# Kernel tuning notes

Hardware: AMD Instinct MI355X
Metric: run time of the kernel (lower is better)

The kernel has to match this reference:

```python
import jax, jax.numpy as jnp
import numpy as np

B, NQ, NM, NHR, D, H, FF = 16, 100, 5440, 4096, 256, 8, 2048

def _ln(x, w, b):
    m = x.mean(-1, keepdims=True)
    v = ((x - m) ** 2).mean(-1, keepdims=True)
    return (x - m) * jax.lax.rsqrt(v + 1e-5) * w + b

def setup_inputs():
    key = jax.random.key(0)
    ks = iter(jax.random.split(key, 32))
    def rn(shape, s=1.0):
        return jax.random.normal(next(ks), shape, jnp.float32) * s
    return {
        'tgt': rn((B, NQ, D)),
        'memory': rn((B, NM, D)),
        'memory_hr': rn((B, NHR, D)),
        'prior_attn_bias': rn((B, NQ, NM)),
        'query_pos': rn((B, NQ, D)),
        'ln_cross_w': jnp.ones((D,)), 'ln_cross_b': jnp.zeros((D,)),
        'q_w': rn((D, D), 0.02), 'q_b': jnp.zeros((D,)),
        'k_w': rn((D, D), 0.02), 'k_b': jnp.zeros((D,)),
        'v_w': rn((D, D), 0.02), 'v_b': jnp.zeros((D,)),
        'out_w': rn((D, D), 0.02), 'out_b': jnp.zeros((D,)),
        'ln_self_w': jnp.ones((D,)), 'ln_self_b': jnp.zeros((D,)),
        'sa_in_w': rn((3 * D, D), 0.02), 'sa_in_b': jnp.zeros((3 * D,)),
        'sa_out_w': rn((D, D), 0.02), 'sa_out_b': jnp.zeros((D,)),
        'ln_ffn_w': jnp.ones((D,)), 'ln_ffn_b': jnp.zeros((D,)),
        'lin1_w': rn((FF, D), 0.02), 'lin1_b': jnp.zeros((FF,)),
        'lin2_w': rn((D, FF), 0.02), 'lin2_b': jnp.zeros((D,)),
        'me_w': rn((D, D), 0.02), 'me_b': jnp.zeros((D,)),
    }

def reference(tgt, memory, memory_hr, prior_attn_bias, query_pos,
              ln_cross_w, ln_cross_b, q_w, q_b, k_w, k_b, v_w, v_b,
              out_w, out_b, ln_self_w, ln_self_b, sa_in_w, sa_in_b,
              sa_out_w, sa_out_b, ln_ffn_w, ln_ffn_b, lin1_w, lin1_b,
              lin2_w, lin2_b, me_w, me_b):
    b, nq, d = tgt.shape
    nm = memory.shape[1]
    h = H
    dh = d // h
    scale = dh ** -0.5
    # ---- cross-attention with additive prior bias (eval mode: dropout = id) ----
    x = _ln(tgt, ln_cross_w, ln_cross_b)
    q = ((x + query_pos) @ q_w.T + q_b).reshape(b, nq, h, dh)
    k = (memory @ k_w.T + k_b).reshape(b, nm, h, dh)
    v = (memory @ v_w.T + v_b).reshape(b, nm, h, dh)
    attn = jnp.einsum('bqhd,bmhd->bhqm', q, k) * scale + prior_attn_bias[:, None]  # [b,h,nq,nm]
    a = jax.nn.softmax(attn, axis=-1)
    o = jnp.einsum('bhqm,bmhd->bqhd', a, v).reshape(b, nq, d)
    tgt = tgt + (o @ out_w.T + out_b)
    # ---- self-attention (torch nn.MultiheadAttention, batch_first, eval) ----
    z = _ln(tgt, ln_self_w, ln_self_b)
    zq = z + query_pos
    qs = (zq @ sa_in_w[:d].T + sa_in_b[:d]).reshape(b, nq, h, dh)
    ks = (zq @ sa_in_w[d:2 * d].T + sa_in_b[d:2 * d]).reshape(b, nq, h, dh)
    vs = (z @ sa_in_w[2 * d:].T + sa_in_b[2 * d:]).reshape(b, nq, h, dh)
    sattn = jax.nn.softmax(jnp.einsum('bqhd,bmhd->bhqm', qs, ks) * scale, axis=-1)
    so = jnp.einsum('bhqm,bmhd->bqhd', sattn, vs).reshape(b, nq, d)
    tgt = tgt + (so @ sa_out_w.T + sa_out_b)
    # ---- FFN ----
    y = _ln(tgt, ln_ffn_w, ln_ffn_b)
    y = jax.nn.gelu(y @ lin1_w.T + lin1_b, approximate=False) @ lin2_w.T + lin2_b
    tgt = tgt + y
    # ---- mask branch ----
    mask_logits = jnp.einsum('bqd,bmd->bqm', tgt @ me_w.T + me_b, memory_hr)
    return (tgt, mask_logits)
```

## Files before the change

### kernel.cpp

```cpp
#include <hip/hip_runtime.h>

typedef unsigned short u16;
typedef unsigned int u32;
typedef __bf16 bf16x8 __attribute__((ext_vector_type(8)));
typedef float f32x4 __attribute__((ext_vector_type(4)));

__device__ __forceinline__ u16 f2b(float f) {
  u32 u = __float_as_uint(f);
  u32 r = (u + 0x7fffu + ((u >> 16) & 1u)) >> 16;
  return (u16)r;
}
__device__ __forceinline__ float b2f(u16 h) {
  return __uint_as_float(((u32)h) << 16);
}
__device__ __forceinline__ bf16x8 zero8() {
  union { uint4 u; bf16x8 v; } z; z.u = make_uint4(0u, 0u, 0u, 0u); return z.v;
}
__device__ __forceinline__ u32 cvtpk(float lo, float hi) {
  u32 r;
  asm("v_cvt_pk_bf16_f32 %0, %1, %2" : "=v"(r) : "v"(lo), "v"(hi));
  return r;
}

struct Seg { const float* in; u16* out; int n4; };
struct PrepArgs {
  Seg seg[7];
  const float *k_w, *v_w, *k_b, *v_b, *pbias;
  u16 *Wf, *biasT;
  float *kvB;
};

__global__ __launch_bounds__(256)
void prep_kernel(PrepArgs a)
{
  __shared__ float S[100][69];
  const int bx = blockIdx.x, tid = threadIdx.x;
  if (bx < 1472) {
    int bxr = bx;
#pragma unroll
    for (int k = 0; k < 7; ++k) {
      const int nb = a.seg[k].n4 >> 8;
      if (bxr < nb) {
        const int i = bxr * 256 + tid;
        const float4 f = *(const float4*)(a.seg[k].in + (size_t)i * 4);
        uint2 pk; pk.x = cvtpk(f.x, f.y); pk.y = cvtpk(f.z, f.w);
        *(uint2*)(a.seg[k].out + (size_t)i * 4) = pk;
        return;
      }
      bxr -= nb;
    }
    return;
  } else if (bx < 1536) {
    const int i = bx - 1472, gI = i >> 3, ks = i & 7;
    const int nt = tid >> 6, lane = tid & 63, lr = lane & 15, g = lane >> 4;
    const float* src = (gI < 4 ? a.k_w + (size_t)(gI * 64 + nt * 16 + lr) * 256
                               : a.v_w + (size_t)((gI - 4) * 64 + nt * 16 + lr) * 256)
                       + ks * 32 + g * 8;
    const float4 f0 = *(const float4*)src;
    const float4 f1 = *(const float4*)(src + 4);
    uint4 pk;
    pk.x = cvtpk(f0.x, f0.y); pk.y = cvtpk(f0.z, f0.w);
    pk.z = cvtpk(f1.x, f1.y); pk.w = cvtpk(f1.z, f1.w);
    *(uint4*)(a.Wf + (size_t)((gI * 8 + ks) * 4 + nt) * 512 + lane * 8) = pk;
  } else if (bx < 1538) {
    const int i = (bx - 1536) * 256 + tid;
    a.kvB[i] = (i < 256) ? a.k_b[i] : a.v_b[i - 256];
  } else {
    const int bt = bx - 1538;
    const int b = bt / 85, m0 = (bt - b * 85) * 64;
    for (int idx = tid; idx < 1600; idx += 256) {
      const int q = idx >> 4, seg = idx & 15;
      const float4 v = *(const float4*)(a.pbias + (size_t)(b * 100 + q) * 5440 + m0 + seg * 4);
      S[q][seg * 4 + 0] = v.x; S[q][seg * 4 + 1] = v.y;
      S[q][seg * 4 + 2] = v.z; S[q][seg * 4 + 3] = v.w;
    }
    __syncthreads();
    for (int idx = tid; idx < 1792; idx += 256) {
      const int m = idx / 28, qg = (idx % 28) * 4;
      u16 h[4];
#pragma unroll
      for (int r = 0; r < 4; ++r) {
        const int q = qg + r;
        h[r] = (q < 100) ? f2b(S[q][m]) : (u16)0;
      }
      uint2 pk;
      pk.x = (u32)h[0] | ((u32)h[1] << 16);
      pk.y = (u32)h[2] | ((u32)h[3] << 16);
      *(uint2*)(a.biasT + ((size_t)(b * 5440 + m0 + m)) * 112 + qg) = pk;
    }
  }
}

template<int ROWS>
__device__ __forceinline__ void ln_stage(const float* __restrict__ x, int row0,
    const float* __restrict__ w, const float* __restrict__ b,
    const float* __restrict__ pos, u16* As)
{
  const int tid = threadIdx.x, lane = tid & 63, wid = tid >> 6;
  const float4 wv = *(const float4*)(w + lane * 4);
  const float4 bv = *(const float4*)(b + lane * 4);
#pragma unroll
  for (int rr = 0; rr < ROWS / 4; ++rr) {
    const int rl = wid * (ROWS / 4) + rr;
    const size_t o = (size_t)(row0 + rl) * 256 + lane * 4;
    const float4 v = *(const float4*)(x + o);
    float s = v.x + v.y + v.z + v.w;
#pragma unroll
    for (int m = 1; m < 64; m <<= 1) s += __shfl_xor(s, m);
    const float mean = s * (1.f / 256.f);
    const float d0 = v.x - mean, d1 = v.y - mean, d2 = v.z - mean, d3 = v.w - mean;
    float ss = d0 * d0 + d1 * d1 + d2 * d2 + d3 * d3;
#pragma unroll
    for (int m = 1; m < 64; m <<= 1) ss += __shfl_xor(ss, m);
    const float rs = rsqrtf(ss * (1.f / 256.f) + 1e-5f);
    float y0 = d0 * rs * wv.x + bv.x;
    float y1 = d1 * rs * wv.y + bv.y;
    float y2 = d2 * rs * wv.z + bv.z;
    float y3 = d3 * rs * wv.w + bv.w;
    if (pos) {
      const float4 pv = *(const float4*)(pos + o);
      y0 += pv.x; y1 += pv.y; y2 += pv.z; y3 += pv.w;
    }
    uint2 pk; pk.x = cvtpk(y0, y1); pk.y = cvtpk(y2, y3);
    const int byte = (rl * 512 + lane * 8) ^ ((rl & 7) << 4);
    *(uint2*)((char*)As + byte) = pk;
  }
}

__device__ __forceinline__ void gemm16x128(const u16* As, const u16* __restrict__ W,
                                           u16 (*Ws)[40], f32x4 acc[2])
{
  const int tid = threadIdx.x, lane = tid & 63, wid = tid >> 6;
  const int g = lane >> 4, lr = lane & 15;
  for (int k0 = 0; k0 < 256; k0 += 32) {
    for (int cid = tid; cid < 512; cid += 256) {
      const int r = cid >> 2, cg = (cid & 3) * 8;
      *(uint4*)&Ws[r][cg] = *(const uint4*)(W + (size_t)r * 256 + k0 + cg);
    }
    __syncthreads();
    const int abyte = (lr * 512 + k0 * 2 + g * 16) ^ ((lr & 7) << 4);
    const bf16x8 af = *(const bf16x8*)((const char*)As + abyte);
#pragma unroll
    for (int nt = 0; nt < 2; ++nt) {
      const bf16x8 bfr = *(const bf16x8*)&Ws[wid * 32 + nt * 16 + lr][g * 8];
      acc[nt] = __builtin_amdgcn_mfma_f32_16x16x32_bf16(af, bfr, acc[nt], 0, 0, 0);
    }
    __syncthreads();
  }
}

__global__ __launch_bounds__(256)
void qproj_kernel(const float* __restrict__ x, const float* __restrict__ lnw,
                  const float* __restrict__ lnb, const float* __restrict__ pos,
                  const u16* __restrict__ W, const float* __restrict__ bias,
                  u16* __restrict__ out, float scale)
{
  __shared__ u16 As[16 * 256];
  __shared__ u16 Ws[128][40];
  const int tid = threadIdx.x, lane = tid & 63, wid = tid >> 6;
  const int g = lane >> 4, lr = lane & 15;
  const int row0 = blockIdx.x * 16, n0 = blockIdx.y * 128;
  ln_stage<16>(x, row0, lnw, lnb, pos, As);
  f32x4 acc[2] = {};
  gemm16x128(As, W + (size_t)n0 * 256, Ws, acc);
#pragma unroll
  for (int nt = 0; nt < 2; ++nt) {
    const int col = n0 + wid * 32 + nt * 16 + lr;
    const float bv = bias[col];
#pragma unroll
    for (int r = 0; r < 4; ++r) {
      const int row = row0 + g * 4 + r;
      out[(size_t)row * 256 + col] = f2b((acc[nt][r] + bv) * scale);
    }
  }
}

__global__ __launch_bounds__(256)
void sain_kernel(const float* __restrict__ x, const float* __restrict__ lnw,
                 const float* __restrict__ lnb, const float* __restrict__ pos,
                 const u16* __restrict__ W, const float* __restrict__ bias,
                 float* __restrict__ qkb, float* __restrict__ vsb)
{
  __shared__ u16 As[16 * 256];
  __shared__ u16 Ws[128][40];
  const int tid = threadIdx.x, lane = tid & 63, wid = tid >> 6;
  const int g = lane >> 4, lr = lane & 15;
  const int row0 = blockIdx.x * 16, y = blockIdx.y;
  ln_stage<16>(x, row0, lnw, lnb, (y < 4) ? pos : nullptr, As);
  f32x4 acc[2] = {};
  gemm16x128(As, W + (size_t)y * 128 * 256, Ws, acc);
#pragma unroll
  for (int nt = 0; nt < 2; ++nt) {
    const int cl = wid * 32 + nt * 16 + lr;
    const float bv = bias[y * 128 + cl];
#pragma unroll
    for (int r = 0; r < 4; ++r) {
      const int row = row0 + g * 4 + r;
      const float v = acc[nt][r] + bv;
      if (y < 4) qkb[(size_t)row * 512 + y * 128 + cl] = v;
      else       vsb[(size_t)row * 256 + (y - 4) * 128 + cl] = v;
    }
  }
}

__global__ __launch_bounds__(256)
void ffn1_kernel(const float* __restrict__ x, const float* __restrict__ lnw,
                 const float* __restrict__ lnb, const u16* __restrict__ W,
                 const float* __restrict__ bias, u16* __restrict__ out)
{
  __shared__ u16 As[64 * 256];
  __shared__ u16 Ws[256][40];
  const int tid = threadIdx.x, lane = tid & 63, wid = tid >> 6;
  const int g = lane >> 4, lr = lane & 15;
  const int row0 = blockIdx.x * 64, n0 = blockIdx.y * 256;
  ln_stage<64>(x, row0, lnw, lnb, nullptr, As);
  f32x4 acc[16] = {};
  for (int k0 = 0; k0 < 256; k0 += 32) {
    for (int cid = tid; cid < 1024; cid += 256) {
      const int r = cid >> 2, cg = (cid & 3) * 8;
      *(uint4*)&Ws[r][cg] = *(const uint4*)(W + (size_t)(n0 + r) * 256 + k0 + cg);
    }
    __syncthreads();
    const int arow = wid * 16 + lr;
    const int abyte = (arow * 512 + k0 * 2 + g * 16) ^ ((arow & 7) << 4);
    const bf16x8 af = *(const bf16x8*)((const char*)As + abyte);
#pragma unroll
    for (int nt = 0; nt < 16; ++nt) {
      const bf16x8 bfr = *(const bf16x8*)&Ws[nt * 16 + lr][g * 8];
      acc[nt] = __builtin_amdgcn_mfma_f32_16x16x32_bf16(af, bfr, acc[nt], 0, 0, 0);
    }
    __syncthreads();
  }
#pragma unroll
  for (int nt = 0; nt < 16; ++nt) {
    const int col = n0 + nt * 16 + lr;
    const float bv = bias[col];
#pragma unroll
    for (int r = 0; r < 4; ++r) {
      const int row = row0 + wid * 16 + g * 4 + r;
      float v = acc[nt][r] + bv;
      v = 0.5f * v * (1.f + erff(v * 0.70710678118654752f));
      out[(size_t)row * 2048 + col] = f2b(v);
    }
  }
}

template<int BM, int BN, int WM, int WN, int GELU_, int RES_, int OF32, int OBF>
__global__ __launch_bounds__(256)
void gemm_kernel(const u16* __restrict__ Ap, const u16* __restrict__ W,
                 const float* __restrict__ bias, const float* __restrict__ res,
                 float* __restrict__ Cf, u16* __restrict__ Cb,
                 int M, int N, int K, float scale)
{
  constexpr int WROWS = BM / WM;
  constexpr int WCOLS = BN / WN;
  constexpr int MT = WROWS / 16;
  constexpr int NT = WCOLS / 16;
  static_assert(WM * WN == 4, "4 waves");
  __shared__ u16 As[BM][40];
  __shared__ u16 Ws[BN][40];
  const int tid = threadIdx.x, lane = tid & 63, wid = tid >> 6;
  const int g = lane >> 4, lr = lane & 15;
  const int m0 = blockIdx.x * BM, n0 = blockIdx.y * BN;
  const int wm = wid / WN, wn = wid % WN;
  f32x4 acc[MT][NT] = {};
  for (int k0 = 0; k0 < K; k0 += 32) {
    for (int cid = tid; cid < BM * 4; cid += 256) {
      int r = cid >> 2, cg = (cid & 3) * 8;
      *(uint4*)&As[r][cg] = *(const uint4*)(Ap + (size_t)(m0 + r) * K + k0 + cg);
    }
    for (int cid = tid; cid < BN * 4; cid += 256) {
      int r = cid >> 2, cg = (cid & 3) * 8;
      *(uint4*)&Ws[r][cg] = *(const uint4*)(W + (size_t)(n0 + r) * K + k0 + cg);
    }
    __syncthreads();
    bf16x8 af[MT], bfr[NT];
#pragma unroll
    for (int mt = 0; mt < MT; ++mt) af[mt] = *(const bf16x8*)&As[wm * WROWS + mt * 16 + lr][g * 8];
#pragma unroll
    for (int nt = 0; nt < NT; ++nt) bfr[nt] = *(const bf16x8*)&Ws[wn * WCOLS + nt * 16 + lr][g * 8];
#pragma unroll
    for (int mt = 0; mt < MT; ++mt)
#pragma unroll
      for (int nt = 0; nt < NT; ++nt)
        acc[mt][nt] = __builtin_amdgcn_mfma_f32_16x16x32_bf16(af[mt], bfr[nt], acc[mt][nt], 0, 0, 0);
    __syncthreads();
  }
#pragma unroll
  for (int mt = 0; mt < MT; ++mt)
#pragma unroll
    for (int nt = 0; nt < NT; ++nt) {
      const int col = n0 + wn * WCOLS + nt * 16 + lr;
      const float bv = bias[col];
#pragma unroll
      for (int r = 0; r < 4; ++r) {
        const int row = m0 + wm * WROWS + mt * 16 + g * 4 + r;
        float v = (acc[mt][nt][r] + bv) * scale;
        if constexpr (GELU_) v = 0.5f * v * (1.f + erff(v * 0.70710678118654752f));
        if constexpr (RES_) v += res[(size_t)row * N + col];
        if constexpr (OF32) Cf[(size_t)row * N + col] = v;
        if constexpr (OBF) Cb[(size_t)row * N + col] = f2b(v);
      }
    }
}

__global__ __launch_bounds__(512, 4)
void kv_gemm_kernel(const float* __restrict__ A, const u16* __restrict__ Wf,
                    const float* __restrict__ biasKV,
                    u16* __restrict__ Kb, u16* __restrict__ Vt)
{
  __shared__ u16 As[64 * 256];
  const int tid = threadIdx.x, lane = tid & 63, wid = tid >> 6;
  const int g = lane >> 4, lr = lane & 15;
  const int bidx = blockIdx.x / 85, t = blockIdx.x - bidx * 85;
  const int row0 = blockIdx.x * 64;

  for (int ch = tid; ch < 2048; ch += 512) {
    const int r = ch >> 5, c8 = (ch & 31) * 8;
    const float* ap = A + (size_t)(row0 + r) * 256 + c8;
    const float4 f0 = *(const float4*)ap;
    const float4 f1 = *(const float4*)(ap + 4);
    uint4 pk;
    pk.x = cvtpk(f0.x, f0.y);
    pk.y = cvtpk(f0.z, f0.w);
    pk.z = cvtpk(f1.x, f1.y);
    pk.w = cvtpk(f1.z, f1.w);
    const int byte = r * 512 + c8 * 2;
    *(uint4*)((char*)As + (byte ^ ((r & 7) << 4))) = pk;
  }
  __syncthreads();

  const u16* wbase = Wf + (size_t)wid * 8 * 4 * 512 + lane * 8;
  f32x4 acc[4][4] = {};
#pragma unroll 2
  for (int ks = 0; ks < 8; ++ks) {
    bf16x8 bfv[4], af[4];
#pragma unroll
    for (int nt = 0; nt < 4; ++nt)
      bfv[nt] = *(const bf16x8*)(wbase + (ks * 4 + nt) * 512);
#pragma unroll
    for (int mt = 0; mt < 4; ++mt) {
      const int r = mt * 16 + lr;
      const int byte = r * 512 + ks * 64 + g * 16;
      af[mt] = *(const bf16x8*)((const char*)As + (byte ^ ((r & 7) << 4)));
    }
#pragma unroll
    for (int mt = 0; mt < 4; ++mt)
#pragma unroll
      for (int nt = 0; nt < 4; ++nt)
        acc[mt][nt] = __builtin_amdgcn_mfma_f32_16x16x32_bf16(af[mt], bfv[nt], acc[mt][nt], 0, 0, 0);
  }
  __syncthreads();

  const int isV = wid >> 2;
  if (isV) {
#pragma unroll
    for (int nt = 0; nt < 4; ++nt) {
      const int col = (wid - 4) * 64 + nt * 16 + lr;
      const float bv = biasKV[256 + col];
#pragma unroll
      for (int mt = 0; mt < 4; ++mt)
#pragma unroll
        for (int r = 0; r < 4; ++r) {
          const int slot = (mt >> 1) * 32 + 8 * g + 2 * r + (mt & 1);
          const int byte = (col * 128 + slot * 2) ^ ((col & 7) << 4);
          *(u16*)((char*)As + byte) = f2b(acc[mt][nt][r] + bv);
        }
    }
  }
  __syncthreads();
  {
    const size_t vbase = (size_t)bidx * 256 * 5440 + (size_t)t * 64;
#pragma unroll
    for (int p = 0; p < 4; ++p) {
      const int idx = p * 512 + tid;
      const int col = idx >> 3, chunk = idx & 7;
      const int lbyte = col * 128 + ((chunk * 16) ^ ((col & 7) << 4));
      const uint4 v = *(const uint4*)((const char*)As + lbyte);
      *(uint4*)(Vt + vbase + (size_t)col * 5440 + chunk * 8) = v;
    }
  }
  __syncthreads();
  if (!isV) {
#pragma unroll
    for (int nt = 0; nt < 4; ++nt) {
      const int col = wid * 64 + nt * 16 + lr;
      const float bv = biasKV[col];
#pragma unroll
      for (int mt = 0; mt < 4; ++mt)
#pragma unroll
        for (int r = 0; r < 4; ++r) {
          const int row = mt * 16 + g * 4 + r;
          const int byte = (row * 512 + col * 2) ^ ((row & 7) << 4);
          *(u16*)((char*)As + byte) = f2b(acc[mt][nt][r] + bv);
        }
    }
  }
  __syncthreads();
#pragma unroll
  for (int p = 0; p < 4; ++p) {
    const int idx = p * 512 + tid;
    const int row = idx >> 5, c16 = idx & 31;
    const int lbyte = row * 512 + ((c16 * 16) ^ ((row & 7) << 4));
    const uint4 v = *(const uint4*)((const char*)As + lbyte);
    *(uint4*)(Kb + (size_t)(row0 + row) * 256 + c16 * 8) = v;
  }
}

__global__ __launch_bounds__(256, 3)
void cross_attn_kernel(const u16* __restrict__ Q, const u16* __restrict__ Kb,
                       const u16* __restrict__ Vt, const u16* __restrict__ biasT,
                       float* __restrict__ Opart, float* __restrict__ ML)
{
  __shared__ u32 P32[4][112][20];
  const int tid = threadIdx.x, lane = tid & 63, wid = tid >> 6;
  const int g = lane >> 4, lr = lane & 15;
  const int b = blockIdx.y, c = blockIdx.x;
  const int head = blockIdx.z * 4 + wid;
  const int m_base = c * 320;
  const f32x4 zf = {0.f, 0.f, 0.f, 0.f};

  bf16x8 qf[7];
#pragma unroll
  for (int mt = 0; mt < 7; ++mt) {
    int qr = mt * 16 + lr;
    qf[mt] = (qr < 100) ? *(const bf16x8*)&Q[(size_t)(b * 100 + qr) * 256 + head * 32 + g * 8]
                        : zero8();
  }
  float Mst[7];
  f32x4 Lp[7];
  f32x4 Oa[7][2];
#pragma unroll
  for (int mt = 0; mt < 7; ++mt) { Mst[mt] = -1e30f; Lp[mt] = zf; Oa[mt][0] = zf; Oa[mt][1] = zf; }

  for (int s = 0; s < 10; ++s) {
    const int m0 = m_base + s * 32;
    const bf16x8 kf0 = *(const bf16x8*)&Kb[(size_t)(b * 5440 + m0 + lr) * 256 + head * 32 + g * 8];
    const bf16x8 kf1 = *(const bf16x8*)&Kb[(size_t)(b * 5440 + m0 + 16 + lr) * 256 + head * 32 + g * 8];
    const size_t vrow = ((size_t)(b * 8 + head) * 32 + lr) * 5440 + m0 + g * 8;
    const bf16x8 vf0 = *(const bf16x8*)&Vt[vrow];
    const bf16x8 vf1 = *(const bf16x8*)&Vt[vrow + 16 * 5440];
    const u16* bb = biasT + ((size_t)(b * 5440 + m0 + lr)) * 112 + g * 4;
#pragma unroll
    for (int mt = 0; mt < 7; ++mt) {
      f32x4 s0 = __builtin_amdgcn_mfma_f32_16x16x32_bf16(qf[mt], kf0, zf, 0, 0, 0);
      f32x4 s1 = __builtin_amdgcn_mfma_f32_16x16x32_bf16(qf[mt], kf1, zf, 0, 0, 0);
      const uint2 b0 = *(const uint2*)(bb + mt * 16);
      const uint2 b1 = *(const uint2*)(bb + 16 * 112 + mt * 16);
      s0[0] += b2f((u16)b0.x);      s0[1] += b2f((u16)(b0.x >> 16));
      s0[2] += b2f((u16)b0.y);      s0[3] += b2f((u16)(b0.y >> 16));
      s1[0] += b2f((u16)b1.x);      s1[1] += b2f((u16)(b1.x >> 16));
      s1[2] += b2f((u16)b1.y);      s1[3] += b2f((u16)(b1.y >> 16));
      float mx = fmaxf(fmaxf(fmaxf(s0[0], s0[1]), fmaxf(s0[2], s0[3])),
                       fmaxf(fmaxf(s1[0], s1[1]), fmaxf(s1[2], s1[3])));
#pragma unroll
      for (int d = 1; d < 16; d <<= 1) mx = fmaxf(mx, __shfl_xor(mx, d, 16));
      const float newM = fmaxf(Mst[mt], mx);
      const float al = __expf(Mst[mt] - newM);
      Mst[mt] = newM;
      f32x4 p0, p1;
#pragma unroll
      for (int r = 0; r < 4; ++r) {
        p0[r] = __expf(s0[r] - newM);
        p1[r] = __expf(s1[r] - newM);
      }
      Lp[mt] = Lp[mt] * al + (p0 + p1);
      Oa[mt][0] *= al;
      Oa[mt][1] *= al;
#pragma unroll
      for (int r = 0; r < 4; ++r)
        P32[wid][mt * 16 + g * 4 + r][lr] = (u32)f2b(p0[r]) | ((u32)f2b(p1[r]) << 16);
    }
#pragma unroll
    for (int mt = 0; mt < 7; ++mt) {
      const bf16x8 pa = *(const bf16x8*)&P32[wid][mt * 16 + lr][g * 4];
      Oa[mt][0] = __builtin_amdgcn_mfma_f32_16x16x32_bf16(pa, vf0, Oa[mt][0], 0, 0, 0);
      Oa[mt][1] = __builtin_amdgcn_mfma_f32_16x16x32_bf16(pa, vf1, Oa[mt][1], 0, 0, 0);
    }
  }
  const int bh = b * 8 + head;
#pragma unroll
  for (int mt = 0; mt < 7; ++mt)
#pragma unroll
    for (int r = 0; r < 4; ++r) {
      const int qr = mt * 16 + g * 4 + r;
      if (qr < 100) {
        float L = Lp[mt][r];
#pragma unroll
        for (int d = 1; d < 16; d <<= 1) L += __shfl_xor(L, d, 16);
        const size_t rb = (size_t)(bh * 17 + c) * 100 + qr;
        Opart[rb * 32 + lr] = Oa[mt][0][r];
        Opart[rb * 32 + 16 + lr] = Oa[mt][1][r];
        if (lr == 0) { ML[rb * 2] = Mst[mt]; ML[rb * 2 + 1] = L; }
      }
    }
}

__global__ __launch_bounds__(256)
void reduce_attn_kernel(const float* __restrict__ Opart, const float* __restrict__ ML,
                        u16* __restrict__ outb)
{
  const int row = blockIdx.x;
  const int b = row / 100, q = row % 100;
  const int h = threadIdx.x >> 5, d = threadIdx.x & 31;
  const int bh = b * 8 + h;
  float gm = -1e30f;
  for (int c = 0; c < 17; ++c) gm = fmaxf(gm, ML[((size_t)(bh * 17 + c) * 100 + q) * 2]);
  float l = 0.f, o = 0.f;
  for (int c = 0; c < 17; ++c) {
    const size_t rb = (size_t)(bh * 17 + c) * 100 + q;
    const float w = __expf(ML[rb * 2] - gm);
    l += ML[rb * 2 + 1] * w;
    o += Opart[rb * 32 + d] * w;
  }
  outb[(size_t)row * 256 + h * 32 + d] = f2b(o / l);
}

__global__ __launch_bounds__(128)
void self_attn_kernel(const float* __restrict__ qk, const float* __restrict__ vs,
                      u16* __restrict__ so)
{
  __shared__ u16 kk[100][36];
  __shared__ u16 vv[100][36];
  __shared__ float S[100][101];
  const int b = blockIdx.x >> 3, h = blockIdx.x & 7;
  const int t = threadIdx.x;
  for (int e = t; e < 3200; e += 128) {
    const int r = e >> 5, cq = e & 31;
    kk[r][cq] = f2b(qk[(size_t)(b * 100 + r) * 512 + 256 + h * 32 + cq]);
    vv[r][cq] = f2b(vs[(size_t)(b * 100 + r) * 256 + h * 32 + cq]);
  }
  __syncthreads();
  if (t < 100) {
    float qr_[32];
#pragma unroll
    for (int cq = 0; cq < 32; ++cq) qr_[cq] = qk[(size_t)(b * 100 + t) * 512 + h * 32 + cq];
    for (int m = 0; m < 100; ++m) {
      float dp = 0.f;
#pragma unroll
      for (int cq = 0; cq < 32; ++cq) dp += qr_[cq] * b2f(kk[m][cq]);
      S[t][m] = dp * 0.17677669529663687f;
    }
    float mx = -1e30f;
    for (int m = 0; m < 100; ++m) mx = fmaxf(mx, S[t][m]);
    float sum = 0.f;
    for (int m = 0; m < 100; ++m) { const float p = __expf(S[t][m] - mx); S[t][m] = p; sum += p; }
    const float inv = 1.f / sum;
    float o[32];
#pragma unroll
    for (int cq = 0; cq < 32; ++cq) o[cq] = 0.f;
    for (int m = 0; m < 100; ++m) {
      const float p = S[t][m];
#pragma unroll
      for (int cq = 0; cq < 32; ++cq) o[cq] += p * b2f(vv[m][cq]);
    }
#pragma unroll
    for (int cq = 0; cq < 32; ++cq)
      so[(size_t)(b * 100 + t) * 256 + h * 32 + cq] = f2b(o[cq] * inv);
  }
}

__global__ __launch_bounds__(256)
void mask_gemm_kernel(const u16* __restrict__ tm, const float* __restrict__ hr,
                      float* __restrict__ out)
{
  __shared__ u16 As[112][40];
  __shared__ u16 Bs[64][40];
  const int tid = threadIdx.x, lane = tid & 63, wid = tid >> 6;
  const int g = lane >> 4, lr = lane & 15;
  const int b = blockIdx.y, n0 = blockIdx.x * 64;
  f32x4 acc[7] = {};
  for (int k0 = 0; k0 < 256; k0 += 32) {
    for (int cid = tid; cid < 448; cid += 256) {
      const int r = cid >> 2, cg = (cid & 3) * 8;
      uint4 val = {0u, 0u, 0u, 0u};
      if (r < 100) val = *(const uint4*)&tm[(size_t)(b * 100 + r) * 256 + k0 + cg];
      *(uint4*)&As[r][cg] = val;
    }
    {
      const int r = tid >> 2, cg = (tid & 3) * 8;
      const float* hp = hr + (size_t)(b * 4096 + n0 + r) * 256 + k0 + cg;
      float4 f0 = *(const float4*)hp;
      float4 f1 = *(const float4*)(hp + 4);
      uint4 pk;
      pk.x = cvtpk(f0.x, f0.y); pk.y = cvtpk(f0.z, f0.w);
      pk.z = cvtpk(f1.x, f1.y); pk.w = cvtpk(f1.z, f1.w);
      *(uint4*)&Bs[r][cg] = pk;
    }
    __syncthreads();
    const bf16x8 bfr = *(const bf16x8*)&Bs[wid * 16 + lr][g * 8];
#pragma unroll
    for (int mt = 0; mt < 7; ++mt) {
      const bf16x8 af = *(const bf16x8*)&As[mt * 16 + lr][g * 8];
      acc[mt] = __builtin_amdgcn_mfma_f32_16x16x32_bf16(af, bfr, acc[mt], 0, 0, 0);
    }
    __syncthreads();
  }
#pragma unroll
  for (int mt = 0; mt < 7; ++mt)
#pragma unroll
    for (int r = 0; r < 4; ++r) {
      const int qr = mt * 16 + g * 4 + r;
      if (qr < 100)
        out[(size_t)(b * 100 + qr) * 4096 + n0 + wid * 16 + lr] = acc[mt][r];
    }
}

extern "C" void kernel_launch(void* const* d_in, const int* in_sizes, int n_in,
                              void* d_out, int out_size, void* d_ws, size_t ws_size,
                              hipStream_t stream)
{
  (void)in_sizes; (void)n_in; (void)out_size; (void)ws_size;
  const float* tgt      = (const float*)d_in[0];
  const float* memory   = (const float*)d_in[1];
  const float* memhr    = (const float*)d_in[2];
  const float* pbias    = (const float*)d_in[3];
  const float* qpos     = (const float*)d_in[4];
  const float* lncw     = (const float*)d_in[5];
  const float* lncb     = (const float*)d_in[6];
  const float* q_w      = (const float*)d_in[7];
  const float* q_b      = (const float*)d_in[8];
  const float* k_w      = (const float*)d_in[9];
  const float* k_b      = (const float*)d_in[10];
  const float* v_w      = (const float*)d_in[11];
  const float* v_b      = (const float*)d_in[12];
  const float* out_w    = (const float*)d_in[13];
  const float* out_b    = (const float*)d_in[14];
  const float* lnsw     = (const float*)d_in[15];
  const float* lnsb     = (const float*)d_in[16];
  const float* sa_in_w  = (const float*)d_in[17];
  const float* sa_in_b  = (const float*)d_in[18];
  const float* sa_out_w = (const float*)d_in[19];
  const float* sa_out_b = (const float*)d_in[20];
  const float* lnfw     = (const float*)d_in[21];
  const float* lnfb     = (const float*)d_in[22];
  const float* l1w      = (const float*)d_in[23];
  const float* l1b      = (const float*)d_in[24];
  const float* l2w      = (const float*)d_in[25];
  const float* l2b      = (const float*)d_in[26];
  const float* me_w     = (const float*)d_in[27];
  const float* me_b     = (const float*)d_in[28];
  float* outf = (float*)d_out;

  char* ws = (char*)d_ws;
  size_t off = 0;
  auto alloc = [&](size_t bytes) -> void* {
    void* p = ws + off;
    off = (off + bytes + 255) & ~(size_t)255;
    return p;
  };
  u16*   Wf    = (u16*)alloc((size_t)131072 * 2);
  u16*   qW    = (u16*)alloc((size_t)65536 * 2);
  u16*   outW  = (u16*)alloc((size_t)65536 * 2);
  u16*   saW   = (u16*)alloc((size_t)196608 * 2);
  u16*   saoW  = (u16*)alloc((size_t)65536 * 2);
  u16*   l1W   = (u16*)alloc((size_t)524288 * 2);
  u16*   l2W   = (u16*)alloc((size_t)524288 * 2);
  u16*   meW   = (u16*)alloc((size_t)65536 * 2);
  float* kvB   = (float*)alloc((size_t)512 * 4);
  u16*   biasT = (u16*)alloc((size_t)9748480 * 2);
  u16*   Qb    = (u16*)alloc((size_t)409600 * 2);
  u16*   Kb    = (u16*)alloc((size_t)22282240 * 2);
  u16*   Vt    = (u16*)alloc((size_t)22282240 * 2);
  float* Opart = (float*)alloc((size_t)6963200 * 4);
  float* MLp   = (float*)alloc((size_t)435200 * 4);
  u16*   attno = (u16*)alloc((size_t)409600 * 2);
  float* tgt1  = (float*)alloc((size_t)409600 * 4);
  float* qkb   = (float*)alloc((size_t)819200 * 4);
  float* vsb   = (float*)alloc((size_t)409600 * 4);
  u16*   sob   = (u16*)alloc((size_t)409600 * 2);
  float* tgt2  = (float*)alloc((size_t)409600 * 4);
  u16*   hb    = (u16*)alloc((size_t)3276800 * 2);
  u16*   t3b   = (u16*)alloc((size_t)409600 * 2);
  u16*   tmb   = (u16*)alloc((size_t)409600 * 2);

  const float SCALE = 0.17677669529663687f;

  PrepArgs pa;
  pa.seg[0] = {q_w,      qW,   16384};
  pa.seg[1] = {out_w,    outW, 16384};
  pa.seg[2] = {sa_in_w,  saW,  49152};
  pa.seg[3] = {sa_out_w, saoW, 16384};
  pa.seg[4] = {l1w,      l1W,  131072};
  pa.seg[5] = {l2w,      l2W,  131072};
  pa.seg[6] = {me_w,     meW,  16384};
  pa.k_w = k_w; pa.v_w = v_w; pa.k_b = k_b; pa.v_b = v_b; pa.pbias = pbias;
  pa.Wf = Wf; pa.biasT = biasT; pa.kvB = kvB;
  prep_kernel<<<2898, 256, 0, stream>>>(pa);

  qproj_kernel<<<dim3(100, 2), 256, 0, stream>>>(tgt, lncw, lncb, qpos, qW, q_b, Qb, SCALE);
  kv_gemm_kernel<<<dim3(1360), 512, 0, stream>>>(memory, Wf, kvB, Kb, Vt);
  cross_attn_kernel<<<dim3(17, 16, 2), 256, 0, stream>>>(Qb, Kb, Vt, biasT, Opart, MLp);
  reduce_attn_kernel<<<1600, 256, 0, stream>>>(Opart, MLp, attno);
  gemm_kernel<16, 128, 1, 4, 0, 1, 1, 0><<<dim3(100, 2), 256, 0, stream>>>(
      attno, outW, out_b, tgt, tgt1, nullptr, 1600, 256, 256, 1.f);

  sain_kernel<<<dim3(100, 6), 256, 0, stream>>>(tgt1, lnsw, lnsb, qpos, saW, sa_in_b, qkb, vsb);
  self_attn_kernel<<<128, 128, 0, stream>>>(qkb, vsb, sob);
  gemm_kernel<16, 128, 1, 4, 0, 1, 1, 0><<<dim3(100, 2), 256, 0, stream>>>(
      sob, saoW, sa_out_b, tgt1, tgt2, nullptr, 1600, 256, 256, 1.f);

  ffn1_kernel<<<dim3(25, 8), 256, 0, stream>>>(tgt2, lnfw, lnfb, l1W, l1b, hb);
  gemm_kernel<16, 128, 1, 4, 0, 1, 1, 1><<<dim3(100, 2), 256, 0, stream>>>(
      hb, l2W, l2b, tgt2, outf, t3b, 1600, 256, 2048, 1.f);

  gemm_kernel<16, 128, 1, 4, 0, 0, 0, 1><<<dim3(100, 2), 256, 0, stream>>>(
      t3b, meW, me_b, nullptr, nullptr, tmb, 1600, 256, 256, 1.f);
  mask_gemm_kernel<<<dim3(64, 16), 256, 0, stream>>>(tmb, memhr, outf + 409600);
}
```

Baseline: 339.5 us.

## Double cross-attention KV split and overlap V transpose store with K staging

The cross-attention split over the memory dimension goes from 17 to 34 chunks of 160 keys each, doubling the grid so more blocks run concurrently. The reduce kernel and partial buffers grow to match, which adds more partial-output traffic. In the KV GEMM, V results now go to a separate shared buffer with packed 32-bit stores. The V waves write V out to global memory while the K waves stage K in shared memory, which removes two barriers at the cost of 32KB more LDS per block.

New measurement: 343.4 us. Within noise of the previous version (+1.1%).

```diff
diff --git a/kernel.cpp b/kernel.cpp
--- a/kernel.cpp
+++ b/kernel.cpp
@@ -4,6 +4,8 @@
 typedef unsigned int u32;
 typedef __bf16 bf16x8 __attribute__((ext_vector_type(8)));
 typedef float f32x4 __attribute__((ext_vector_type(4)));
+
+#define NCH 34
 
 __device__ __forceinline__ u16 f2b(float f) {
   u32 u = __float_as_uint(f);
@@ -310,6 +312,7 @@
                     u16* __restrict__ Kb, u16* __restrict__ Vt)
 {
   __shared__ u16 As[64 * 256];
+  __shared__ u16 Vs[256 * 64];
   const int tid = threadIdx.x, lane = tid & 63, wid = tid >> 6;
   const int g = lane >> 4, lr = lane & 15;
   const int bidx = blockIdx.x / 85, t = blockIdx.x - bidx * 85;
@@ -350,7 +353,6 @@
       for (int nt = 0; nt < 4; ++nt)
         acc[mt][nt] = __builtin_amdgcn_mfma_f32_16x16x32_bf16(af[mt], bfv[nt], acc[mt][nt], 0, 0, 0);
   }
-  __syncthreads();
 
   const int isV = wid >> 2;
   if (isV) {
@@ -359,28 +361,17 @@
       const int col = (wid - 4) * 64 + nt * 16 + lr;
       const float bv = biasKV[256 + col];
 #pragma unroll
-      for (int mt = 0; mt < 4; ++mt)
+      for (int a = 0; a < 2; ++a)
 #pragma unroll
         for (int r = 0; r < 4; ++r) {
-          const int slot = (mt >> 1) * 32 + 8 * g + 2 * r + (mt & 1);
-          const int byte = (col * 128 + slot * 2) ^ ((col & 7) << 4);
-          *(u16*)((char*)As + byte) = f2b(acc[mt][nt][r] + bv);
+          const u32 val = cvtpk(acc[2 * a][nt][r] + bv, acc[2 * a + 1][nt][r] + bv);
+          const int byte = (col * 128 + a * 64 + g * 16 + r * 4) ^ ((col & 7) << 4);
+          *(u32*)((char*)Vs + byte) = val;
         }
     }
   }
   __syncthreads();
-  {
-    const size_t vbase = (size_t)bidx * 256 * 5440 + (size_t)t * 64;
-#pragma unroll
-    for (int p = 0; p < 4; ++p) {
-      const int idx = p * 512 + tid;
-      const int col = idx >> 3, chunk = idx & 7;
-      const int lbyte = col * 128 + ((chunk * 16) ^ ((col & 7) << 4));
-      const uint4 v = *(const uint4*)((const char*)As + lbyte);
-      *(uint4*)(Vt + vbase + (size_t)col * 5440 + chunk * 8) = v;
-    }
-  }
-  __syncthreads();
+
   if (!isV) {
 #pragma unroll
     for (int nt = 0; nt < 4; ++nt) {
@@ -389,11 +380,24 @@
 #pragma unroll
       for (int mt = 0; mt < 4; ++mt)
 #pragma unroll
-        for (int r = 0; r < 4; ++r) {
-          const int row = mt * 16 + g * 4 + r;
-          const int byte = (row * 512 + col * 2) ^ ((row & 7) << 4);
-          *(u16*)((char*)As + byte) = f2b(acc[mt][nt][r] + bv);
+        for (int r = 0; r < 4; r += 2) {
+          const u32 pk = cvtpk(acc[mt][nt][r] + bv, acc[mt][nt][r + 1] + bv);
+          const int rowA = mt * 16 + g * 4 + r;
+          const int rowB = rowA + 1;
+          *(u16*)((char*)As + ((rowA * 512 + col * 2) ^ ((rowA & 7) << 4))) = (u16)pk;
+          *(u16*)((char*)As + ((rowB * 512 + col * 2) ^ ((rowB & 7) << 4))) = (u16)(pk >> 16);
         }
+    }
+  } else {
+    const size_t vbase = (size_t)bidx * 256 * 5440 + (size_t)t * 64;
+    const int t2 = tid - 256;
+#pragma unroll
+    for (int p = 0; p < 8; ++p) {
+      const int idx = p * 256 + t2;
+      const int col = idx >> 3, chunk = idx & 7;
+      const int lbyte = col * 128 + ((chunk * 16) ^ ((col & 7) << 4));
+      const uint4 v = *(const uint4*)((const char*)Vs + lbyte);
+      *(uint4*)(Vt + vbase + (size_t)col * 5440 + chunk * 8) = v;
     }
   }
   __syncthreads();
@@ -417,7 +421,7 @@
   const int g = lane >> 4, lr = lane & 15;
   const int b = blockIdx.y, c = blockIdx.x;
   const int head = blockIdx.z * 4 + wid;
-  const int m_base = c * 320;
+  const int m_base = c * (5440 / NCH);
   const f32x4 zf = {0.f, 0.f, 0.f, 0.f};
 
   bf16x8 qf[7];
@@ -433,7 +437,7 @@
 #pragma unroll
   for (int mt = 0; mt < 7; ++mt) { Mst[mt] = -1e30f; Lp[mt] = zf; Oa[mt][0] = zf; Oa[mt][1] = zf; }
 
-  for (int s = 0; s < 10; ++s) {
+  for (int s = 0; s < (5440 / NCH) / 32; ++s) {
     const int m0 = m_base + s * 32;
     const bf16x8 kf0 = *(const bf16x8*)&Kb[(size_t)(b * 5440 + m0 + lr) * 256 + head * 32 + g * 8];
     const bf16x8 kf1 = *(const bf16x8*)&Kb[(size_t)(b * 5440 + m0 + 16 + lr) * 256 + head * 32 + g * 8];
@@ -488,7 +492,7 @@
         float L = Lp[mt][r];
 #pragma unroll
         for (int d = 1; d < 16; d <<= 1) L += __shfl_xor(L, d, 16);
-        const size_t rb = (size_t)(bh * 17 + c) * 100 + qr;
+        const size_t rb = (size_t)(bh * NCH + c) * 100 + qr;
         Opart[rb * 32 + lr] = Oa[mt][0][r];
         Opart[rb * 32 + 16 + lr] = Oa[mt][1][r];
         if (lr == 0) { ML[rb * 2] = Mst[mt]; ML[rb * 2 + 1] = L; }
@@ -505,10 +509,10 @@
   const int h = threadIdx.x >> 5, d = threadIdx.x & 31;
   const int bh = b * 8 + h;
   float gm = -1e30f;
-  for (int c = 0; c < 17; ++c) gm = fmaxf(gm, ML[((size_t)(bh * 17 + c) * 100 + q) * 2]);
+  for (int c = 0; c < NCH; ++c) gm = fmaxf(gm, ML[((size_t)(bh * NCH + c) * 100 + q) * 2]);
   float l = 0.f, o = 0.f;
-  for (int c = 0; c < 17; ++c) {
-    const size_t rb = (size_t)(bh * 17 + c) * 100 + q;
+  for (int c = 0; c < NCH; ++c) {
+    const size_t rb = (size_t)(bh * NCH + c) * 100 + q;
     const float w = __expf(ML[rb * 2] - gm);
     l += ML[rb * 2 + 1] * w;
     o += Opart[rb * 32 + d] * w;
@@ -662,8 +666,8 @@
   u16*   Qb    = (u16*)alloc((size_t)409600 * 2);
   u16*   Kb    = (u16*)alloc((size_t)22282240 * 2);
   u16*   Vt    = (u16*)alloc((size_t)22282240 * 2);
-  float* Opart = (float*)alloc((size_t)6963200 * 4);
-  float* MLp   = (float*)alloc((size_t)435200 * 4);
+  float* Opart = (float*)alloc((size_t)(128 * NCH * 100 * 32) * 4);
+  float* MLp   = (float*)alloc((size_t)(128 * NCH * 100 * 2) * 4);
   u16*   attno = (u16*)alloc((size_t)409600 * 2);
   float* tgt1  = (float*)alloc((size_t)409600 * 4);
   float* qkb   = (float*)alloc((size_t)819200 * 4);
@@ -690,7 +694,7 @@
 
   qproj_kernel<<<dim3(100, 2), 256, 0, stream>>>(tgt, lncw, lncb, qpos, qW, q_b, Qb, SCALE);
   kv_gemm_kernel<<<dim3(1360), 512, 0, stream>>>(memory, Wf, kvB, Kb, Vt);
-  cross_attn_kernel<<<dim3(17, 16, 2), 256, 0, stream>>>(Qb, Kb, Vt, biasT, Opart, MLp);
+  cross_attn_kernel<<<dim3(NCH, 16, 2), 256, 0, stream>>>(Qb, Kb, Vt, biasT, Opart, MLp);
   reduce_attn_kernel<<<1600, 256, 0, stream>>>(Opart, MLp, attno);
   gemm_kernel<16, 128, 1, 4, 0, 1, 1, 0><<<dim3(100, 2), 256, 0, stream>>>(
       attno, outW, out_b, tgt, tgt1, nullptr, 1600, 256, 256, 1.f);
```
